# Performance work log

Measured on AMD Instinct MI355X. Metric: run time of the kernel, lower is better.

The kernel has to match this reference:

```python
import jax, jax.numpy as jnp
import numpy as np

B, N, M, C, K = 4, 4096, 4096, 64, 32
RADIUS = 0.1
EPS = 1e-5


def setup_inputs() -> dict:
    key = jax.random.key(0)
    ks = jax.random.split(key, 32)
    inp = {
        "query_xyz": jax.random.uniform(ks[0], (B, N, 3), jnp.float32),
        "support_xyz": jax.random.uniform(ks[1], (B, M, 3), jnp.float32),
        "query_mask": jax.random.randint(ks[2], (B, N), 0, 2, jnp.int32),
        "support_mask": jax.random.randint(ks[3], (B, M), 0, 2, jnp.int32),
        "support_features": jax.random.normal(ks[4], (B, C, M), jnp.float32),
    }
    names = ["theta1", "theta2", "phi", "psi", "alpha", "gamma1", "gamma2"]
    in_ch = {"theta1": 3}
    for j, nm in enumerate(names):
        inp[f"W_{nm}"] = jax.random.normal(ks[5 + j], (C, in_ch.get(nm, C)), jnp.float32) * 0.05
        inp[f"b_{nm}"] = jax.random.normal(ks[12 + j], (C,), jnp.float32) * 0.05
    for j, nm in enumerate(["theta", "gamma"]):
        inp[f"g_{nm}"] = 1.0 + 0.1 * jax.random.normal(ks[19 + 2 * j], (C,), jnp.float32)
        inp[f"be_{nm}"] = 0.1 * jax.random.normal(ks[20 + 2 * j], (C,), jnp.float32)
        inp[f"rm_{nm}"] = jnp.zeros((C,), jnp.float32)
        inp[f"rv_{nm}"] = jnp.ones((C,), jnp.float32)
    return inp


def _conv(W, b, x):
    # 1x1 Conv2d: channelwise linear on [B, C_in, N, K]
    return jnp.einsum('oc,bcnk->bonk', W, x) + b[None, :, None, None]


def _bn(x, g, be, rm, rv):
    # BatchNorm2d, inference form with running stats
    inv = g / jnp.sqrt(rv + EPS)
    return x * inv[None, :, None, None] + (be - rm * inv)[None, :, None, None]


def _forward(query_xyz, support_xyz, query_mask, support_mask, support_features, P):
    Bq, Nq = query_xyz.shape[:2]
    # pairwise squared distances [B, N, M]; masked support pushed to +inf
    d2 = jnp.sum((query_xyz[:, :, None, :] - support_xyz[:, None, :, :]) ** 2, axis=-1)
    d2 = jnp.where(support_mask[:, None, :] > 0, d2, jnp.inf)
    # ball query as K-nearest-within-radius
    neg, idx = jax.lax.top_k(-d2, K)                    # idx: [B, N, K]
    nbr_mask = (-neg) <= RADIUS ** 2                    # valid-neighbor mask
    flat = idx.reshape(Bq, Nq * K)
    x_j = jnp.take_along_axis(support_features, flat[:, None, :], axis=2).reshape(Bq, -1, Nq, K)
    g_xyz = jnp.take_along_axis(support_xyz, flat[:, :, None], axis=1).reshape(Bq, Nq, K, 3)
    # normalize_xyz=True -> offsets divided by radius; layout [B, 3, N, K]
    pos = ((g_xyz - query_xyz[:, :, None, :]) / RADIUS).transpose(0, 3, 1, 2)
    # nearest-neighbor query for x_i [B, C, N]
    idx_nn = jnp.argmin(d2, axis=-1)
    x_i = jnp.take_along_axis(support_features, idx_nn[:, None, :], axis=2)
    # positional encoding delta
    delta = jax.nn.relu(_bn(_conv(P['W_theta2'], P['b_theta2'],
                                  _conv(P['W_theta1'], P['b_theta1'], pos)),
                            P['g_theta'], P['be_theta'], P['rm_theta'], P['rv_theta']))
    lin_i = _conv(P['W_phi'], P['b_phi'], x_i[..., None])   # [B,C,N,1], broadcast over K
    lin_j = _conv(P['W_psi'], P['b_psi'], x_j)
    rel = lin_i - lin_j + delta
    rel = jax.nn.relu(_bn(_conv(P['W_gamma2'], P['b_gamma2'],
                                _conv(P['W_gamma1'], P['b_gamma1'], rel)),
                          P['g_gamma'], P['be_gamma'], P['rm_gamma'], P['rv_gamma']))
    weights = jax.nn.softmax(rel, axis=-1)                   # softmax over neighbor axis
    feats = _conv(P['W_alpha'], P['b_alpha'], x_j) + delta
    fmask = nbr_mask.astype(feats.dtype) + (1.0 - query_mask.astype(feats.dtype))[:, :, None]
    feats = feats * fmask[:, None, :, :]
    return jnp.sum(weights * feats, axis=-1)                 # [B, C, N]


def reference(query_xyz, support_xyz, query_mask, support_mask, support_features,
              W_theta1, b_theta1, W_theta2, b_theta2, W_phi, b_phi, W_psi, b_psi,
              W_alpha, b_alpha, W_gamma1, b_gamma1, W_gamma2, b_gamma2,
              g_theta, be_theta, rm_theta, rv_theta, g_gamma, be_gamma, rm_gamma, rv_gamma):
    P = dict(locals())
    return _forward(query_xyz, support_xyz, query_mask, support_mask, support_features, P)
```

## Files before the change

### kernel.cpp

```cpp
#include <hip/hip_runtime.h>
#include <cstdint>
#include <cstddef>

#define NN 4096
#define MM 4096
#define CC 64
#define KK 32
#define INF_F __builtin_huge_valf()

#define SC 2304
#define CCAP 2560
#define NBUCK 256

typedef __bf16 bf16x8 __attribute__((ext_vector_type(8)));
typedef __bf16 bf16x4 __attribute__((ext_vector_type(4)));
typedef float f32x16 __attribute__((ext_vector_type(16)));

#define NFRAG 40
#define NPRE 24
#define ASTRIDE 68
#define ESTRIDE 36

#define WFENCE() asm volatile("s_waitcnt lgkmcnt(0)")


__device__ __forceinline__ f32x16 zero16() {
  f32x16 z;
#pragma unroll
  for (int i = 0; i < 16; ++i) z[i] = 0.0f;
  return z;
}

__device__ __forceinline__ void conv1(const bf16x8* Wr, int conv,
                                      const bf16x8* B4, f32x16& a0, f32x16& a1) {
#pragma unroll
  for (int s = 0; s < 4; ++s) {
    a0 = __builtin_amdgcn_mfma_f32_32x32x16_bf16(Wr[(conv * 2 + 0) * 4 + s], B4[s], a0, 0, 0, 0);
    a1 = __builtin_amdgcn_mfma_f32_32x32x16_bf16(Wr[(conv * 2 + 1) * 4 + s], B4[s], a1, 0, 0, 0);
  }
}

__device__ __forceinline__ void conv1g(const bf16x8* __restrict__ Wf, int conv, int lane,
                                       const bf16x8* B4, f32x16& a0, f32x16& a1) {
#pragma unroll
  for (int s = 0; s < 4; ++s) {
    const bf16x8 w0 = Wf[((conv * 2 + 0) * 4 + s) * 64 + lane];
    const bf16x8 w1 = Wf[((conv * 2 + 1) * 4 + s) * 64 + lane];
    a0 = __builtin_amdgcn_mfma_f32_32x32x16_bf16(w0, B4[s], a0, 0, 0, 0);
    a1 = __builtin_amdgcn_mfma_f32_32x32x16_bf16(w1, B4[s], a1, 0, 0, 0);
  }
}

__device__ __forceinline__ void sort64(float& v, int& i, int lane) {
#pragma unroll
  for (int k = 2; k <= 64; k <<= 1) {
#pragma unroll
    for (int j = k >> 1; j > 0; j >>= 1) {
      const float ov = __shfl_xor(v, j);
      const int oi = __shfl_xor(i, j);
      const bool up = ((lane & k) == 0);
      const bool lower = ((lane & j) == 0);
      const bool take = (up == lower) ? (ov < v) : (ov > v);
      if (take) { v = ov; i = oi; }
    }
  }
}

__device__ __forceinline__ void insert_cands(float vv, int ii, float& sv, int& si,
                                             float& cmax, int lane) {
  unsigned long long cand = __ballot(vv < cmax);
  while (cand) {
    const int src = __ffsll((unsigned long long)cand) - 1;
    cand &= cand - 1;
    const float dc = __shfl(vv, src);
    if (dc < cmax) {
      const int im = __shfl(ii, src);
      const float up_s = __shfl_up(sv, 1);
      const int up_i = __shfl_up(si, 1);
      const bool pg = sv > dc;
      const bool pgu = (lane > 0) && (up_s > dc);
      const float ns = pg ? (pgu ? up_s : dc) : sv;
      const int ni = pg ? (pgu ? up_i : im) : si;
      if (lane < 32) { sv = ns; si = ni; }
      cmax = __shfl(sv, 31);
    }
  }
}

__global__ void pt_setup(const float* __restrict__ sf, const float* __restrict__ sxyz,
                         const int* __restrict__ smask,
                         const float* __restrict__ Wpsi, const float* __restrict__ W2,
                         const float* __restrict__ Wg1, const float* __restrict__ Wg2,
                         const float* __restrict__ Wa, const float* __restrict__ Wphi,
                         const float* __restrict__ gT, const float* __restrict__ beT,
                         const float* __restrict__ rmT, const float* __restrict__ rvT,
                         const float* __restrict__ gG, const float* __restrict__ beG,
                         const float* __restrict__ rmG, const float* __restrict__ rvG,
                         const float* __restrict__ b2, const float* __restrict__ bg1,
                         const float* __restrict__ bg2, const float* __restrict__ ba,
                         __bf16* __restrict__ ftb, float4* __restrict__ sx4,
                         __bf16* __restrict__ Wpack, float* __restrict__ WphiT,
                         float4* __restrict__ eo, float4* __restrict__ bo,
                         int* __restrict__ cnt2) {
  const int blk = blockIdx.x;
  const int tid = threadIdx.x;

  if (blk < 256) {
    const int b = blk >> 6;
    const int m = ((blk & 63) << 6) + (tid & 63);
    const int cg = tid >> 6;
    float v[16];
#pragma unroll
    for (int j = 0; j < 16; ++j) v[j] = sf[((size_t)(b * CC + cg * 16 + j)) * MM + m];
    __bf16* db = ftb + ((size_t)(b * MM + m)) * CC + cg * 16;
    bf16x8 t0, t1;
#pragma unroll
    for (int j = 0; j < 8; ++j) { t0[j] = (__bf16)v[j]; t1[j] = (__bf16)v[8 + j]; }
    *(bf16x8*)db = t0;
    *(bf16x8*)(db + 8) = t1;
    if (cg == 0) {
      const size_t g = (size_t)(b * MM + m);
      sx4[g] = make_float4(sxyz[g * 3 + 0], sxyz[g * 3 + 1], sxyz[g * 3 + 2], 0.0f);
    }
    return;
  }

  if (blk < 320) {
    __shared__ int hcnt[NBUCK];
    const int sub = blk - 256;
    const int b = sub >> 4;
    const int s = sub & 15;
    hcnt[tid] = 0;
    __syncthreads();
    const int m = s * 256 + tid;
    const size_t g = (size_t)b * MM + m;
    if (smask[g] > 0) {
      int bk = (int)(sxyz[g * 3 + 0] * 256.0f);
      bk = min(max(bk, 0), NBUCK - 1);
      atomicAdd(&hcnt[bk], 1);
    }
    __syncthreads();
    cnt2[(b * 16 + s) * NBUCK + tid] = hcnt[tid];
    return;
  }

  const int t = (blk - 320) * 256 + tid;
  if (t < NFRAG * 64) {
    const int lane = t & 63;
    const int fi = t >> 6;
    const int s = fi & 3;
    const int mt = (fi >> 2) & 1;
    const int conv = fi >> 3;
    const float* W = conv == 0 ? Wpsi : conv == 1 ? W2 : conv == 2 ? Wg1 : conv == 3 ? Wg2 : Wa;
    const int m = mt * 32 + (lane & 31);
    const int k0 = s * 16 + (lane >> 5) * 8;
    bf16x8 vh;
#pragma unroll
    for (int j = 0; j < 8; ++j) vh[j] = (__bf16)W[m * CC + k0 + j];
    ((bf16x8*)Wpack)[fi * 64 + lane] = vh;
    return;
  }
  const int t2 = t - NFRAG * 64;
  if (t2 < CC * CC) {
    WphiT[t2] = Wphi[(t2 & 63) * CC + (t2 >> 6)];
    return;
  }
  const int o = t2 - CC * CC;
  if (o < CC) {
    const float invT = gT[o] / sqrtf(rvT[o] + 1e-5f);
    const float invG = gG[o] / sqrtf(rvG[o] + 1e-5f);
    eo[o] = make_float4(invT, beT[o] - rmT[o] * invT, invG, beG[o] - rmG[o] * invG);
    bo[o] = make_float4(b2[o], bg1[o], bg2[o], ba[o]);
  }
}

__global__ void pt_scan(int* __restrict__ cnt2, int* __restrict__ boffp,
                        float4* __restrict__ cpts) {
  __shared__ int wtot[4];
  const int b = blockIdx.x;
  const int tid = threadIdx.x;
  const int lane = tid & 63;
  const int w = tid >> 6;

  int c[16];
  int tot = 0;
#pragma unroll
  for (int s = 0; s < 16; ++s) {
    c[s] = cnt2[(b * 16 + s) * NBUCK + tid];
    tot += c[s];
  }
  int inc = tot;
#pragma unroll
  for (int off = 1; off < 64; off <<= 1) {
    const int o = __shfl_up(inc, off);
    if (lane >= off) inc += o;
  }
  if (lane == 63) wtot[w] = inc;
  __syncthreads();
  int excl = inc - tot;
#pragma unroll
  for (int i = 0; i < 4; ++i) excl += (i < w) ? wtot[i] : 0;
  boffp[b * 257 + tid] = excl;
  const int total = wtot[0] + wtot[1] + wtot[2] + wtot[3];
  if (tid == 0) boffp[b * 257 + 256] = total;
  int base = excl;
#pragma unroll
  for (int s = 0; s < 16; ++s) {
    cnt2[(b * 16 + s) * NBUCK + tid] = base;
    base += c[s];
  }
  float4* dst = cpts + (size_t)b * CCAP;
  for (int i = total + tid; i < SC; i += 256)
    dst[i] = make_float4(1e4f, 1e4f, 1e4f, __int_as_float(0));
}

__global__ void pt_scatter(const float* __restrict__ sxyz, const int* __restrict__ smask,
                           const int* __restrict__ cnt2, float4* __restrict__ cpts) {
  __shared__ int cur[NBUCK];
  const int b = blockIdx.x >> 4;
  const int s = blockIdx.x & 15;
  const int tid = threadIdx.x;
  cur[tid] = cnt2[(b * 16 + s) * NBUCK + tid];
  __syncthreads();
  const int m = s * 256 + tid;
  const size_t g = (size_t)b * MM + m;
  if (smask[g] > 0) {
    const float x = sxyz[g * 3 + 0];
    const float y = sxyz[g * 3 + 1];
    const float z = sxyz[g * 3 + 2];
    int bk = (int)(x * 256.0f);
    bk = min(max(bk, 0), NBUCK - 1);
    const int pos = atomicAdd(&cur[bk], 1);
    cpts[(size_t)b * CCAP + pos] = make_float4(x, y, z, __int_as_float(m));
  }
}

__global__ void pt_knn(const float* __restrict__ qxyz, const float4* __restrict__ cpts,
                       const int* __restrict__ boff, const __bf16* __restrict__ ftb,
                       const float* __restrict__ WphiT, const float* __restrict__ bphi,
                       const float* __restrict__ bpsi,
                       int* __restrict__ oidx, unsigned* __restrict__ ovalid,
                       float* __restrict__ lin) {
  const int lane = threadIdx.x & 63;
  const int qi = blockIdx.x * 4 + (threadIdx.x >> 6);
  const int b = qi >> 12;
  const float qx = qxyz[qi * 3 + 0];
  const float qy = qxyz[qi * 3 + 1];
  const float qz = qxyz[qi * 3 + 2];
  const float4* sb = cpts + (size_t)b * CCAP;
  const int* bo = boff + b * 257;
  const int cnt = bo[256];

  float R = 0.155f;
#pragma unroll
  for (int it = 0; it < 2; ++it) {
    const float cx = fminf(qx + R, 1.0f) - fmaxf(qx - R, 0.0f);
    const float cy = fminf(qy + R, 1.0f) - fmaxf(qy - R, 0.0f);
    const float cz = fminf(qz + R, 1.0f) - fmaxf(qz - R, 0.0f);
    const float n = fmaxf((float)cnt * 0.5235988f * cx * cy * cz, 1.0f);
    R *= __powf(48.0f / n, 0.33333333f);
  }
  R = fminf(fmaxf(R, 0.06f), 0.7f);

  const int lob = max((int)((qx - R) * 256.0f), 0);
  const int hib = min((int)((qx + R) * 256.0f), NBUCK - 1);
  const int r0 = bo[lob] >> 6;
  const int r1 = (bo[hib + 1] + 63) >> 6;

  float v0 = INF_F, v1 = INF_F, v2 = INF_F, v3 = INF_F;
  int i0 = 0, i1 = 0, i2 = 0, i3 = 0;
  int r = r0;
#pragma unroll 1
  for (; r + 4 <= r1; r += 4) {
    float4 P[4];
#pragma unroll
    for (int u = 0; u < 4; ++u) P[u] = sb[(r + u) * 64 + lane];
#pragma unroll
    for (int u = 0; u < 4; ++u) {
      const float dx = P[u].x - qx, dy = P[u].y - qy, dz = P[u].z - qz;
      const float d = dx * dx + dy * dy + dz * dz;
      const int m = __float_as_int(P[u].w);
      const bool c3 = d < v3, c2 = d < v2, c1 = d < v1, c0 = d < v0;
      v3 = c3 ? (c2 ? v2 : d) : v3;  i3 = c3 ? (c2 ? i2 : m) : i3;
      v2 = c2 ? (c1 ? v1 : d) : v2;  i2 = c2 ? (c1 ? i1 : m) : i2;
      v1 = c1 ? (c0 ? v0 : d) : v1;  i1 = c1 ? (c0 ? i0 : m) : i1;
      v0 = c0 ? d : v0;              i0 = c0 ? m : i0;
    }
  }
#pragma unroll 1
  for (; r < r1; ++r) {
    const float4 p = sb[r * 64 + lane];
    const float dx = p.x - qx, dy = p.y - qy, dz = p.z - qz;
    const float d = dx * dx + dy * dy + dz * dz;
    const int m = __float_as_int(p.w);
    const bool c3 = d < v3, c2 = d < v2, c1 = d < v1, c0 = d < v0;
    v3 = c3 ? (c2 ? v2 : d) : v3;  i3 = c3 ? (c2 ? i2 : m) : i3;
    v2 = c2 ? (c1 ? v1 : d) : v2;  i2 = c2 ? (c1 ? i1 : m) : i2;
    v1 = c1 ? (c0 ? v0 : d) : v1;  i1 = c1 ? (c0 ? i0 : m) : i1;
    v0 = c0 ? d : v0;              i0 = c0 ? m : i0;
  }

  float sv = v0;
  int si = i0;
  sort64(sv, si, lane);
  float cmax = __shfl(sv, 31);
  insert_cands(v1, i1, sv, si, cmax, lane);
  insert_cands(v2, i2, sv, si, cmax, lane);
  insert_cands(v3, i3, sv, si, cmax, lane);

  if (__ballot(v3 < cmax) && r1 > r0) {
    {
      const float4 p = sb[r0 * 64 + lane];
      const float dx = p.x - qx, dy = p.y - qy, dz = p.z - qz;
      float v = dx * dx + dy * dy + dz * dz;
      int id = __float_as_int(p.w);
      sort64(v, id, lane);
      sv = v; si = id;
    }
    cmax = __shfl(sv, 31);
    for (int rr = r0 + 1; rr < r1; ++rr) {
      const float4 p = sb[rr * 64 + lane];
      const float dx = p.x - qx, dy = p.y - qy, dz = p.z - qz;
      const float d = dx * dx + dy * dy + dz * dz;
      insert_cands(d, __float_as_int(p.w), sv, si, cmax, lane);
    }
  }

  const float gl = (lob > 0) ? (qx - (float)lob * 0.00390625f) : INF_F;
  const float gr = (hib < NBUCK - 1) ? ((float)(hib + 1) * 0.00390625f - qx) : INF_F;
  const float G = fminf(gl, gr);
  if (cmax > G * G) {
    const float R1 = sqrtf(cmax);
    const int lob2 = max((int)((qx - R1) * 256.0f), 0);
    const int hib2 = min((int)((qx + R1) * 256.0f), NBUCK - 1);
    const int s0 = bo[lob2] >> 6;
    const int s1 = (bo[hib2 + 1] + 63) >> 6;
    for (int rr = s0; rr < r0; ++rr) {
      const float4 p = sb[rr * 64 + lane];
      const float dx = p.x - qx, dy = p.y - qy, dz = p.z - qz;
      insert_cands(dx * dx + dy * dy + dz * dz, __float_as_int(p.w), sv, si, cmax, lane);
    }
    for (int rr = r1; rr < s1; ++rr) {
      const float4 p = sb[rr * 64 + lane];
      const float dx = p.x - qx, dy = p.y - qy, dz = p.z - qz;
      insert_cands(dx * dx + dy * dy + dz * dz, __float_as_int(p.w), sv, si, cmax, lane);
    }
  }

  if (lane < 32) oidx[(size_t)qi * KK + lane] = si;
  const unsigned long long vb = __ballot((lane < 32) && (sv <= 0.01f));
  if (lane == 0) ovalid[qi] = (unsigned)(vb & 0xffffffffull);

  const int nnb = __shfl(si, 0);
  const bf16x8* xr = (const bf16x8*)(ftb + ((size_t)(b * MM + nnb)) * CC);
  float a = bphi[lane] - bpsi[lane];
#pragma unroll
  for (int i = 0; i < 8; ++i) {
    const bf16x8 xv = xr[i];
#pragma unroll
    for (int j = 0; j < 8; ++j) a += WphiT[(8 * i + j) * CC + lane] * (float)xv[j];
  }
  lin[qi * CC + lane] = a;
}

__launch_bounds__(256, 3)
__global__ void pt_fused(
    const float* __restrict__ qxyz, const float4* __restrict__ sx4,
    const int* __restrict__ qmask, const __bf16* __restrict__ ftb,
    const int* __restrict__ kidx, const unsigned* __restrict__ kvalid,
    const float* __restrict__ lin,
    const float* __restrict__ W1, const float* __restrict__ b1,
    const __bf16* __restrict__ Wpack, const float4* __restrict__ eo,
    const float4* __restrict__ bo, float* __restrict__ out) {
  __shared__ float EPI[4][CC * ESTRIDE];
  __shared__ float4 sEO[CC], sBO[CC];
  const int wid = threadIdx.x >> 6;
  const int lane = threadIdx.x & 63;
  const int g = lane >> 5;
  const int col = lane & 31;
  const int q = blockIdx.x * 4 + wid;
  const int b = q >> 12;
  const int nq = q & (NN - 1);
  float* epi = EPI[wid];
  __bf16* act = (__bf16*)epi;
  const bf16x8* Wf = (const bf16x8*)Wpack;

  bf16x8 Wr[NPRE];
#pragma unroll
  for (int f = 0; f < NPRE; ++f) Wr[f] = Wf[f * 64 + lane];

  sEO[lane] = eo[lane];
  sBO[lane] = bo[lane];

  const int idx = kidx[q * KK + col];
  const float fm = (float)((kvalid[q] >> col) & 1u) + 1.0f - (float)qmask[q];

  bf16x8 Xb[4];
  {
    const __bf16* ftq = ftb + ((size_t)(b * MM + idx)) * CC;
#pragma unroll
    for (int s = 0; s < 4; ++s) Xb[s] = *(const bf16x8*)(ftq + s * 16 + g * 8);
  }

  bf16x8 Tb[4];
  {
    const float qx = qxyz[q * 3 + 0], qy = qxyz[q * 3 + 1], qz = qxyz[q * 3 + 2];
    const float4 pj = sx4[(size_t)b * MM + idx];
    const float p0 = (pj.x - qx) * 10.0f;
    const float p1 = (pj.y - qy) * 10.0f;
    const float p2 = (pj.z - qz) * 10.0f;
#pragma unroll
    for (int s = 0; s < 4; ++s) {
      bf16x8 t;
#pragma unroll
      for (int j = 0; j < 8; ++j) {
        const int c = s * 16 + g * 8 + j;
        t[j] = (__bf16)(b1[c] + W1[c * 3 + 0] * p0 + W1[c * 3 + 1] * p1 + W1[c * 3 + 2] * p2);
      }
      Tb[s] = t;
    }
  }
  WFENCE();

  float DELv[32];
  {
    f32x16 aT0 = zero16(), aT1 = zero16();
    conv1(Wr, 1, Tb, aT0, aT1);
#pragma unroll
    for (int mt = 0; mt < 2; ++mt)
#pragma unroll
      for (int t = 0; t < 4; ++t)
#pragma unroll
        for (int i = 0; i < 4; ++i) {
          const int r = t * 4 + i;
          const int o = mt * 32 + 8 * t + 4 * g + i;
          const float4 e = sEO[o];
          DELv[mt * 16 + r] = fmaxf(((mt ? aT1[r] : aT0[r]) + sBO[o].x) * e.x + e.y, 0.0f);
        }
  }

  {
    f32x16 aP0 = zero16(), aP1 = zero16();
    conv1(Wr, 0, Xb, aP0, aP1);
#pragma unroll
    for (int mt = 0; mt < 2; ++mt)
#pragma unroll
      for (int t = 0; t < 4; ++t) {
        const int ob = mt * 32 + 8 * t + 4 * g;
        const float4 lv = *(const float4*)(lin + q * CC + ob);
        const float lva[4] = {lv.x, lv.y, lv.z, lv.w};
        bf16x4 w;
#pragma unroll
        for (int i = 0; i < 4; ++i) {
          const int r = t * 4 + i;
          w[i] = (__bf16)(lva[i] - (mt ? aP1[r] : aP0[r]) + DELv[mt * 16 + r]);
        }
        *(bf16x4*)(act + col * ASTRIDE + ob) = w;
      }
  }
  WFENCE();

  {
    bf16x8 Rb[4];
#pragma unroll
    for (int s = 0; s < 4; ++s) {
      const bf16x4 lo = *(const bf16x4*)(act + col * ASTRIDE + s * 16 + g * 8);
      const bf16x4 hi = *(const bf16x4*)(act + col * ASTRIDE + s * 16 + g * 8 + 4);
      Rb[s] = bf16x8{lo[0], lo[1], lo[2], lo[3], hi[0], hi[1], hi[2], hi[3]};
    }
    f32x16 a0 = zero16(), a1 = zero16();
    conv1(Wr, 2, Rb, a0, a1);
#pragma unroll
    for (int mt = 0; mt < 2; ++mt)
#pragma unroll
      for (int t = 0; t < 4; ++t) {
        const int ob = mt * 32 + 8 * t + 4 * g;
        bf16x4 w;
#pragma unroll
        for (int i = 0; i < 4; ++i) {
          const int r = t * 4 + i;
          w[i] = (__bf16)((mt ? a1[r] : a0[r]) + sBO[ob + i].y);
        }
        *(bf16x4*)(act + col * ASTRIDE + ob) = w;
      }
  }
  WFENCE();

  f32x16 h0 = zero16(), h1 = zero16();
  {
    bf16x8 Rb[4];
#pragma unroll
    for (int s = 0; s < 4; ++s) {
      const bf16x4 lo = *(const bf16x4*)(act + col * ASTRIDE + s * 16 + g * 8);
      const bf16x4 hi = *(const bf16x4*)(act + col * ASTRIDE + s * 16 + g * 8 + 4);
      Rb[s] = bf16x8{lo[0], lo[1], lo[2], lo[3], hi[0], hi[1], hi[2], hi[3]};
    }
    conv1g(Wf, 3, lane, Rb, h0, h1);
  }
  WFENCE();

#pragma unroll
  for (int mt = 0; mt < 2; ++mt)
#pragma unroll
    for (int t = 0; t < 4; ++t)
#pragma unroll
      for (int i = 0; i < 4; ++i) {
        const int r = t * 4 + i;
        const int o = mt * 32 + 4 * g + 8 * t + i;
        const float4 e = sEO[o];
        const float v = fmaxf(((mt ? h1[r] : h0[r]) + sBO[o].z) * e.z + e.w, 0.0f);
        epi[o * ESTRIDE + col] = v;
      }
  WFENCE();

  float ev[32];
  float sum;
  {
    const float* row = epi + lane * ESTRIDE;
    float mx = -INF_F;
#pragma unroll
    for (int n = 0; n < 32; n += 4) {
      const float4 t = *(const float4*)(row + n);
      ev[n] = t.x; ev[n + 1] = t.y; ev[n + 2] = t.z; ev[n + 3] = t.w;
      mx = fmaxf(mx, fmaxf(fmaxf(t.x, t.y), fmaxf(t.z, t.w)));
    }
    sum = 0.0f;
#pragma unroll
    for (int n = 0; n < 32; ++n) { ev[n] = __expf(ev[n] - mx); sum += ev[n]; }
  }
  WFENCE();

  f32x16 fa0 = zero16(), fa1 = zero16();
  conv1g(Wf, 4, lane, Xb, fa0, fa1);

#pragma unroll
  for (int mt = 0; mt < 2; ++mt)
#pragma unroll
    for (int t = 0; t < 4; ++t)
#pragma unroll
      for (int i = 0; i < 4; ++i) {
        const int r = t * 4 + i;
        const int o = mt * 32 + 4 * g + 8 * t + i;
        const float f = ((mt ? fa1[r] : fa0[r]) + sBO[o].w + DELv[mt * 16 + r]) * fm;
        epi[o * ESTRIDE + col] = f;
      }
  WFENCE();

  {
    const float* row = epi + lane * ESTRIDE;
    float acc = 0.0f;
#pragma unroll
    for (int n = 0; n < 32; n += 4) {
      const float4 t = *(const float4*)(row + n);
      acc += ev[n] * t.x + ev[n + 1] * t.y + ev[n + 2] * t.z + ev[n + 3] * t.w;
    }
    out[((size_t)(b * CC + lane)) * NN + nq] = acc * __builtin_amdgcn_rcpf(sum);
  }
}

extern "C" void kernel_launch(void* const* d_in, const int* in_sizes, int n_in,
                              void* d_out, int out_size, void* d_ws, size_t ws_size,
                              hipStream_t stream) {
  (void)in_sizes; (void)n_in; (void)out_size; (void)ws_size;
  const float* qxyz = (const float*)d_in[0];
  const float* sxyz = (const float*)d_in[1];
  const int* qmask = (const int*)d_in[2];
  const int* smask = (const int*)d_in[3];
  const float* sfeat = (const float*)d_in[4];
  const float* W1 = (const float*)d_in[5];
  const float* b1 = (const float*)d_in[6];
  const float* W2 = (const float*)d_in[7];
  const float* b2 = (const float*)d_in[8];
  const float* Wphi = (const float*)d_in[9];
  const float* bphi = (const float*)d_in[10];
  const float* Wpsi = (const float*)d_in[11];
  const float* bpsi = (const float*)d_in[12];
  const float* Wa = (const float*)d_in[13];
  const float* ba = (const float*)d_in[14];
  const float* Wg1 = (const float*)d_in[15];
  const float* bg1 = (const float*)d_in[16];
  const float* Wg2 = (const float*)d_in[17];
  const float* bg2 = (const float*)d_in[18];
  const float* gT = (const float*)d_in[19];
  const float* beT = (const float*)d_in[20];
  const float* rmT = (const float*)d_in[21];
  const float* rvT = (const float*)d_in[22];
  const float* gG = (const float*)d_in[23];
  const float* beG = (const float*)d_in[24];
  const float* rmG = (const float*)d_in[25];
  const float* rvG = (const float*)d_in[26];

  char* ws = (char*)d_ws;
  int* kidx      = (int*)(ws + 0);
  unsigned* kval = (unsigned*)(ws + 2097152);
  __bf16* ftb    = (__bf16*)(ws + 2162688);
  float4* sx4    = (float4*)(ws + 4259840);
  float* lin     = (float*)(ws + 4521984);
  __bf16* Wpack  = (__bf16*)(ws + 8716288);
  float4* eo     = (float4*)(ws + 8757248);
  float4* bo     = (float4*)(ws + 8758272);
  float4* cpts   = (float4*)(ws + 8759296);
  float* WphiT   = (float*)(ws + 8923136);
  int* boffp     = (int*)(ws + 8939520);
  int* cnt2      = (int*)(ws + 8943744);

  hipLaunchKernelGGL(pt_setup, dim3(347), dim3(256), 0, stream,
                     sfeat, sxyz, smask,
                     Wpsi, W2, Wg1, Wg2, Wa, Wphi,
                     gT, beT, rmT, rvT, gG, beG, rmG, rvG, b2, bg1, bg2, ba,
                     ftb, sx4, Wpack, WphiT, eo, bo, cnt2);
  hipLaunchKernelGGL(pt_scan, dim3(4), dim3(256), 0, stream, cnt2, boffp, cpts);
  hipLaunchKernelGGL(pt_scatter, dim3(64), dim3(256), 0, stream, sxyz, smask, cnt2, cpts);
  hipLaunchKernelGGL(pt_knn, dim3(4096), dim3(256), 0, stream,
                     qxyz, cpts, boffp, ftb, WphiT, bphi, bpsi, kidx, kval, lin);
  hipLaunchKernelGGL(pt_fused, dim3(4096), dim3(256), 0, stream,
                     qxyz, sx4, qmask, ftb, kidx, kval, lin,
                     W1, b1, Wpack, eo, bo, (float*)d_out);
}
```

Before: 225.3 us.

## Recompute delta instead of holding it live, raise occupancy to 4 blocks

Drops the 32-float DELv array that stayed live across the whole fused kernel. The delta conv (theta2 + BN + ReLU) is now folded into the MFMA accumulators before the psi/alpha convs and recomputed later from Tb for the alpha path. The launch bound goes from 3 to 4 blocks per CU to use the freed registers for occupancy. The cost is an extra 64x64 conv per query tile and a possible change in bf16 rounding order.

```diff
diff --git a/kernel.cpp b/kernel.cpp
--- a/kernel.cpp
+++ b/kernel.cpp
@@ -363,7 +363,7 @@
   lin[qi * CC + lane] = a;
 }
 
-__launch_bounds__(256, 3)
+__launch_bounds__(256, 4)
 __global__ void pt_fused(
     const float* __restrict__ qxyz, const float4* __restrict__ sx4,
     const int* __restrict__ qmask, const __bf16* __restrict__ ftb,
@@ -422,12 +422,12 @@
   }
   WFENCE();
 
-  float DELv[32];
-  {
-    f32x16 aT0 = zero16(), aT1 = zero16();
-    conv1(Wr, 1, Tb, aT0, aT1);
-#pragma unroll
-    for (int mt = 0; mt < 2; ++mt)
+  {
+    f32x16 a0 = zero16(), a1 = zero16();
+    conv1(Wr, 1, Tb, a0, a1);
+#pragma unroll
+    for (int mt = 0; mt < 2; ++mt) {
+      f32x16& aa = mt ? a1 : a0;
 #pragma unroll
       for (int t = 0; t < 4; ++t)
 #pragma unroll
@@ -435,15 +435,13 @@
           const int r = t * 4 + i;
           const int o = mt * 32 + 8 * t + 4 * g + i;
           const float4 e = sEO[o];
-          DELv[mt * 16 + r] = fmaxf(((mt ? aT1[r] : aT0[r]) + sBO[o].x) * e.x + e.y, 0.0f);
+          aa[r] = -fmaxf((aa[r] + sBO[o].x) * e.x + e.y, 0.0f);
         }
-  }
-
-  {
-    f32x16 aP0 = zero16(), aP1 = zero16();
-    conv1(Wr, 0, Xb, aP0, aP1);
-#pragma unroll
-    for (int mt = 0; mt < 2; ++mt)
+    }
+    conv1(Wr, 0, Xb, a0, a1);
+#pragma unroll
+    for (int mt = 0; mt < 2; ++mt) {
+      f32x16& aa = mt ? a1 : a0;
 #pragma unroll
       for (int t = 0; t < 4; ++t) {
         const int ob = mt * 32 + 8 * t + 4 * g;
@@ -451,12 +449,10 @@
         const float lva[4] = {lv.x, lv.y, lv.z, lv.w};
         bf16x4 w;
 #pragma unroll
-        for (int i = 0; i < 4; ++i) {
-          const int r = t * 4 + i;
-          w[i] = (__bf16)(lva[i] - (mt ? aP1[r] : aP0[r]) + DELv[mt * 16 + r]);
-        }
+        for (int i = 0; i < 4; ++i) w[i] = (__bf16)(lva[i] - aa[t * 4 + i]);
         *(bf16x4*)(act + col * ASTRIDE + ob) = w;
       }
+    }
   }
   WFENCE();
 
@@ -471,22 +467,20 @@
     f32x16 a0 = zero16(), a1 = zero16();
     conv1(Wr, 2, Rb, a0, a1);
 #pragma unroll
-    for (int mt = 0; mt < 2; ++mt)
+    for (int mt = 0; mt < 2; ++mt) {
+      f32x16& aa = mt ? a1 : a0;
 #pragma unroll
       for (int t = 0; t < 4; ++t) {
         const int ob = mt * 32 + 8 * t + 4 * g;
         bf16x4 w;
 #pragma unroll
-        for (int i = 0; i < 4; ++i) {
-          const int r = t * 4 + i;
-          w[i] = (__bf16)((mt ? a1[r] : a0[r]) + sBO[ob + i].y);
-        }
+        for (int i = 0; i < 4; ++i) w[i] = (__bf16)(aa[t * 4 + i] + sBO[ob + i].y);
         *(bf16x4*)(act + col * ASTRIDE + ob) = w;
       }
+    }
   }
   WFENCE();
 
-  f32x16 h0 = zero16(), h1 = zero16();
   {
     bf16x8 Rb[4];
 #pragma unroll
@@ -495,22 +489,23 @@
       const bf16x4 hi = *(const bf16x4*)(act + col * ASTRIDE + s * 16 + g * 8 + 4);
       Rb[s] = bf16x8{lo[0], lo[1], lo[2], lo[3], hi[0], hi[1], hi[2], hi[3]};
     }
+    f32x16 h0 = zero16(), h1 = zero16();
     conv1g(Wf, 3, lane, Rb, h0, h1);
-  }
-  WFENCE();
-
-#pragma unroll
-  for (int mt = 0; mt < 2; ++mt)
-#pragma unroll
-    for (int t = 0; t < 4; ++t)
-#pragma unroll
-      for (int i = 0; i < 4; ++i) {
-        const int r = t * 4 + i;
-        const int o = mt * 32 + 4 * g + 8 * t + i;
-        const float4 e = sEO[o];
-        const float v = fmaxf(((mt ? h1[r] : h0[r]) + sBO[o].z) * e.z + e.w, 0.0f);
-        epi[o * ESTRIDE + col] = v;
-      }
+    WFENCE();
+#pragma unroll
+    for (int mt = 0; mt < 2; ++mt) {
+      f32x16& hh = mt ? h1 : h0;
+#pragma unroll
+      for (int t = 0; t < 4; ++t)
+#pragma unroll
+        for (int i = 0; i < 4; ++i) {
+          const int o = mt * 32 + 4 * g + 8 * t + i;
+          const float4 e = sEO[o];
+          epi[o * ESTRIDE + col] =
+              fmaxf((hh[t * 4 + i] + sBO[o].z) * e.z + e.w, 0.0f);
+        }
+    }
+  }
   WFENCE();
 
   float ev[32];
@@ -530,20 +525,35 @@
   }
   WFENCE();
 
-  f32x16 fa0 = zero16(), fa1 = zero16();
-  conv1g(Wf, 4, lane, Xb, fa0, fa1);
-
-#pragma unroll
-  for (int mt = 0; mt < 2; ++mt)
-#pragma unroll
-    for (int t = 0; t < 4; ++t)
-#pragma unroll
-      for (int i = 0; i < 4; ++i) {
-        const int r = t * 4 + i;
-        const int o = mt * 32 + 4 * g + 8 * t + i;
-        const float f = ((mt ? fa1[r] : fa0[r]) + sBO[o].w + DELv[mt * 16 + r]) * fm;
-        epi[o * ESTRIDE + col] = f;
-      }
+  {
+    f32x16 a0 = zero16(), a1 = zero16();
+    conv1g(Wf, 1, lane, Tb, a0, a1);
+#pragma unroll
+    for (int mt = 0; mt < 2; ++mt) {
+      f32x16& aa = mt ? a1 : a0;
+#pragma unroll
+      for (int t = 0; t < 4; ++t)
+#pragma unroll
+        for (int i = 0; i < 4; ++i) {
+          const int r = t * 4 + i;
+          const int o = mt * 32 + 8 * t + 4 * g + i;
+          const float4 e = sEO[o];
+          aa[r] = fmaxf((aa[r] + sBO[o].x) * e.x + e.y, 0.0f) + sBO[o].w;
+        }
+    }
+    conv1g(Wf, 4, lane, Xb, a0, a1);
+#pragma unroll
+    for (int mt = 0; mt < 2; ++mt) {
+      f32x16& aa = mt ? a1 : a0;
+#pragma unroll
+      for (int t = 0; t < 4; ++t)
+#pragma unroll
+        for (int i = 0; i < 4; ++i) {
+          const int o = mt * 32 + 4 * g + 8 * t + i;
+          epi[o * ESTRIDE + col] = aa[t * 4 + i] * fm;
+        }
+    }
+  }
   WFENCE();
 
   {
```

Measured after the change: 318.9 us. +41.5%, slower.
